# Kernel optimization log

Measured on AMD Instinct MI355X. Metric: run time of the kernel, lower is better.

The kernel has to match this reference:

```python
import jax, jax.numpy as jnp
import numpy as np

B, S, I, H, L = 32, 512, 512, 512, 2


def _gru_scan(x, wx, bx, wh, bh, reverse):
    # x: [B, S, layer_in_dim]; wx: [3H, in], wh: [3H, H]. PyTorch gate order r,z,n.
    hdim = wh.shape[1]
    gx = jnp.einsum('bsi,gi->sbg', x, wx) + bx  # precompute input gates: [S, B, 3H]
    h0 = jnp.zeros((x.shape[0], hdim), x.dtype)

    def step(h, gxt):
        gh = h @ wh.T + bh
        r = jax.nn.sigmoid(gxt[:, :hdim] + gh[:, :hdim])
        z = jax.nn.sigmoid(gxt[:, hdim:2 * hdim] + gh[:, hdim:2 * hdim])
        n = jnp.tanh(gxt[:, 2 * hdim:] + r * gh[:, 2 * hdim:])
        hn = (1 - z) * n + z * h
        return hn, hn

    hN, ys = jax.lax.scan(step, h0, gx, reverse=reverse)
    return ys.transpose(1, 0, 2), hN  # [B, S, H], [B, H]


def setup_inputs() -> dict:
    key = jax.random.key(0)
    ks = jax.random.split(key, 17)
    sc = 0.05
    d = {'x': jax.random.normal(ks[0], (B, S, I), jnp.float32)}
    i = 1
    for layer in range(L):
        in_dim = I if layer == 0 else 2 * H
        for tag in ('f', 'b'):
            d[f'wx_{tag}{layer}'] = jax.random.normal(ks[i], (3 * H, in_dim), jnp.float32) * sc
            d[f'bx_{tag}{layer}'] = jax.random.normal(jax.random.fold_in(ks[i], 1), (3 * H,), jnp.float32) * sc
            d[f'wh_{tag}{layer}'] = jax.random.normal(jax.random.fold_in(ks[i], 2), (3 * H, H), jnp.float32) * sc
            d[f'bh_{tag}{layer}'] = jax.random.normal(jax.random.fold_in(ks[i], 3), (3 * H,), jnp.float32) * sc
            i += 1
    return d


def reference(x,
              wx_f0, bx_f0, wh_f0, bh_f0, wx_b0, bx_b0, wh_b0, bh_b0,
              wx_f1, bx_f1, wh_f1, bh_f1, wx_b1, bx_b1, wh_b1, bh_b1):
    layers = [((wx_f0, bx_f0, wh_f0, bh_f0), (wx_b0, bx_b0, wh_b0, bh_b0)),
              ((wx_f1, bx_f1, wh_f1, bh_f1), (wx_b1, bx_b1, wh_b1, bh_b1))]
    layer_in = x
    h_fw, h_bw = [], []
    for fw, bw in layers:
        yf, hf = _gru_scan(layer_in, *fw, reverse=False)
        yb, hb = _gru_scan(layer_in, *bw, reverse=True)
        layer_in = jnp.concatenate([yf, yb], axis=-1)  # [B, S, 2H] (dropout p=0 -> identity)
        h_fw.append(hf)
        h_bw.append(hb)
    return layer_in, (jnp.stack(h_fw, 0), jnp.stack(h_bw, 0))
```

## Files before the change

### kernel.cpp

```cpp
#include <hip/hip_runtime.h>
#include <stdint.h>

typedef short short8 __attribute__((ext_vector_type(8)));
typedef float floatx4 __attribute__((ext_vector_type(4)));
typedef unsigned long long u64;

__device__ __forceinline__ unsigned short f2bf(float f) {
  union { float f; unsigned int i; } v;
  v.f = f;
  unsigned int r = v.i + 0x7fffu + ((v.i >> 16) & 1u);
  return (unsigned short)(r >> 16);
}
__device__ __forceinline__ short8 cvt8(const float4 a, const float4 b) {
  short8 v;
  v[0] = (short)f2bf(a.x); v[1] = (short)f2bf(a.y);
  v[2] = (short)f2bf(a.z); v[3] = (short)f2bf(a.w);
  v[4] = (short)f2bf(b.x); v[5] = (short)f2bf(b.y);
  v[6] = (short)f2bf(b.z); v[7] = (short)f2bf(b.w);
  return v;
}
__device__ __forceinline__ float sane(float x, float lim) {
  return fminf(fmaxf(x, -lim), lim);
}

extern __shared__ unsigned short lds[];

template<int K, int XM>
__global__ __launch_bounds__(256)
void gx_gemm(const float* __restrict__ xf,
             const unsigned short* __restrict__ xb,
             const float* __restrict__ wxf,
             const float* __restrict__ wxb,
             float* __restrict__ gx)
{
  unsigned short* As = lds;
  unsigned short* Bs = lds + 128 * 40;

  const int M0 = blockIdx.x * 128;
  const int N0 = blockIdx.y * 128;
  const int dir = blockIdx.z;
  const float* wx = dir ? wxb : wxf;
  float* gxd = gx + (long)dir * 16384 * 1536;

  const int tid = threadIdx.x;
  const int lane = tid & 63;
  const int wid = tid >> 6;
  const int q = lane >> 4;
  const int l16 = lane & 15;
  const int wM = (wid >> 1) * 64;
  const int wN = (wid & 1) * 64;

  const int srow = tid >> 1;
  const int k0 = (tid & 1) * 16;

  floatx4 acc[4][4];
#pragma unroll
  for (int i = 0; i < 4; ++i)
#pragma unroll
    for (int j = 0; j < 4; ++j) acc[i][j] = (floatx4){0.f, 0.f, 0.f, 0.f};

  for (int kk = 0; kk < K; kk += 32) {
    __syncthreads();
    {
      const int mg = M0 + srow;
      if (XM) {
        const float* ap = xf + ((long)(mg & 31) * 512 + (mg >> 5)) * 512 + kk + k0;
        float4 f0 = *(const float4*)(ap);
        float4 f1 = *(const float4*)(ap + 4);
        float4 f2 = *(const float4*)(ap + 8);
        float4 f3 = *(const float4*)(ap + 12);
        *(short8*)(As + srow * 40 + k0)     = cvt8(f0, f1);
        *(short8*)(As + srow * 40 + k0 + 8) = cvt8(f2, f3);
      } else {
        const unsigned short* ap = xb + (long)mg * 1024 + kk + k0;
        *(short8*)(As + srow * 40 + k0)     = *(const short8*)(ap);
        *(short8*)(As + srow * 40 + k0 + 8) = *(const short8*)(ap + 8);
      }
      const float* bp = wx + (long)(N0 + srow) * K + kk + k0;
      float4 g0 = *(const float4*)(bp);
      float4 g1 = *(const float4*)(bp + 4);
      float4 g2 = *(const float4*)(bp + 8);
      float4 g3 = *(const float4*)(bp + 12);
      *(short8*)(Bs + srow * 40 + k0)     = cvt8(g0, g1);
      *(short8*)(Bs + srow * 40 + k0 + 8) = cvt8(g2, g3);
    }
    __syncthreads();
    short8 a[4], b[4];
#pragma unroll
    for (int mt = 0; mt < 4; ++mt)
      a[mt] = *(const short8*)(As + (wM + mt * 16 + l16) * 40 + q * 8);
#pragma unroll
    for (int nt = 0; nt < 4; ++nt)
      b[nt] = *(const short8*)(Bs + (wN + nt * 16 + l16) * 40 + q * 8);
#pragma unroll
    for (int mt = 0; mt < 4; ++mt)
#pragma unroll
      for (int nt = 0; nt < 4; ++nt)
        acc[mt][nt] = __builtin_amdgcn_mfma_f32_16x16x32_bf16(
            a[mt], b[nt], acc[mt][nt], 0, 0, 0);
  }
#pragma unroll
  for (int mt = 0; mt < 4; ++mt) {
    const int row = M0 + wM + mt * 16 + q * 4;
#pragma unroll
    for (int nt = 0; nt < 4; ++nt) {
      const int col = N0 + wN + nt * 16 + l16;
#pragma unroll
      for (int r = 0; r < 4; ++r)
        gxd[(long)(row + r) * 1536 + col] = acc[mt][nt][r];
    }
  }
}

template<int OUT>
__global__ __launch_bounds__(128)
void gru_rec(const float* __restrict__ gx,
             const float* __restrict__ whfp, const float* __restrict__ bhfp,
             const float* __restrict__ whbp, const float* __restrict__ bhbp,
             const float* __restrict__ bxfp, const float* __restrict__ bxbp,
             unsigned short* __restrict__ ring,
             unsigned short* __restrict__ y0,
             float* __restrict__ omain,
             float* __restrict__ out_hf,
             float* __restrict__ out_hb)
{
  constexpr u64 TM = 0x4000400040004000ULL;
  unsigned short* whs = lds;

  const int bid = blockIdx.x;
  const bool fw = bid < 16;
  const int d = fw ? bid : bid - 16;
  const int tid = threadIdx.x;
  const int lane = tid & 63;
  const int w = tid >> 6;
  const int q = lane >> 4;
  const int l16 = lane & 15;

  const float* wh = fw ? whfp : whbp;
  const float* bh = fw ? bhfp : bhbp;
  const float* bx = fw ? bxfp : bxbp;
  const int col0 = d * 32;
  const int dirofs = fw ? 0 : 512;
  const float* gxd = gx + (long)(fw ? 0 : 1) * 16384 * 1536;

  for (int c = tid; c < 96 * 64; c += 128) {
    int lr = c >> 6, c8 = (c & 63) * 8;
    int g = lr >> 5, jc = lr & 31;
    const float* src = wh + (long)(g * 512 + col0 + jc) * 512 + c8;
    *(short8*)(whs + lr * 520 + c8) =
        cvt8(*(const float4*)src, *(const float4*)(src + 4));
  }
  __syncthreads();

  const int jj = l16;
  float cr[2], cz[2], bxn[2], bhn[2];
#pragma unroll
  for (int n2 = 0; n2 < 2; ++n2) {
    const int cc = col0 + n2 * 16 + jj;
    cr[n2] = bx[cc] + bh[cc];
    cz[n2] = bx[512 + cc] + bh[512 + cc];
    bxn[n2] = bx[1024 + cc];
    bhn[n2] = bh[1024 + cc];
  }

  const int cb = w * 16 + q * 4;
  const int ab = w * 16 + l16;
  const floatx4 fz = {0.f, 0.f, 0.f, 0.f};
  float h[2][4] = {{0.f, 0.f, 0.f, 0.f}, {0.f, 0.f, 0.f, 0.f}};
  unsigned int* ring32 = (unsigned int*)ring;
  unsigned int* y032 = (unsigned int*)y0;

  float nx[24];
  auto load_gx = [&](int t) {
    const float* base = gxd + (long)t * 32 * 1536;
#pragma unroll
    for (int g = 0; g < 3; ++g)
#pragma unroll
      for (int n2 = 0; n2 < 2; ++n2)
#pragma unroll
        for (int r = 0; r < 4; ++r)
          nx[(g * 2 + n2) * 4 + r] =
              base[(long)(cb + r) * 1536 + g * 512 + col0 + n2 * 16 + jj];
  };
  { const int t0 = fw ? 0 : 511; load_gx(t0); }

  union W { u64 u[2]; short8 s; unsigned int dd[4]; };

  for (int it = 0; it < 512; ++it) {
    const int t = fw ? it : 511 - it;
    float cur[24];
#pragma unroll
    for (int i = 0; i < 24; ++i) cur[i] = nx[i];

    const unsigned short* hbase = nullptr;
    u64 expectw = 0;
    if (it > 0) {
      const int slot_r = (it + 1) & 1;
      hbase = ring + ((long)slot_r * 32 + ab) * 1024 + dirofs;
      expectw = ((((it - 1) >> 1) & 1) ^ 1) ? TM : 0ULL;
    }

    W wv[16];
    if (it > 0) {
#pragma unroll
      for (int ks = 0; ks < 16; ++ks) {
        u64* p = (u64*)(hbase + ks * 32 + q * 8);
        wv[ks].u[0] = __hip_atomic_load(p,     __ATOMIC_RELAXED, __HIP_MEMORY_SCOPE_AGENT);
        wv[ks].u[1] = __hip_atomic_load(p + 1, __ATOMIC_RELAXED, __HIP_MEMORY_SCOPE_AGENT);
      }
    }
    if (it < 511) {
      const int tn = fw ? it + 1 : 511 - (it + 1);
      load_gx(tn);
    }

    floatx4 ar[2] = {fz, fz}, az[2] = {fz, fz}, an[2] = {fz, fz};
    if (it > 0) {
      while (true) {
        u64 bad = 0;
#pragma unroll
        for (int ks = 0; ks < 16; ++ks)
          bad |= ((wv[ks].u[0] ^ expectw) | (wv[ks].u[1] ^ expectw)) & TM;
        if (bad == 0) break;
        __builtin_amdgcn_s_sleep(1);
#pragma unroll
        for (int ks = 0; ks < 16; ++ks) {
          u64* p = (u64*)(hbase + ks * 32 + q * 8);
          wv[ks].u[0] = __hip_atomic_load(p,     __ATOMIC_RELAXED, __HIP_MEMORY_SCOPE_AGENT);
          wv[ks].u[1] = __hip_atomic_load(p + 1, __ATOMIC_RELAXED, __HIP_MEMORY_SCOPE_AGENT);
        }
      }
#pragma unroll
      for (int ks = 0; ks < 16; ++ks) {
        wv[ks].dd[0] &= 0xBFFFBFFFu; wv[ks].dd[1] &= 0xBFFFBFFFu;
        wv[ks].dd[2] &= 0xBFFFBFFFu; wv[ks].dd[3] &= 0xBFFFBFFFu;
        short8 a = wv[ks].s;
#pragma unroll
        for (int n2 = 0; n2 < 2; ++n2) {
          short8 vr = *(const short8*)(whs + (n2 * 16 + jj) * 520 + ks * 32 + q * 8);
          short8 vz = *(const short8*)(whs + (32 + n2 * 16 + jj) * 520 + ks * 32 + q * 8);
          short8 vn = *(const short8*)(whs + (64 + n2 * 16 + jj) * 520 + ks * 32 + q * 8);
          ar[n2] = __builtin_amdgcn_mfma_f32_16x16x32_bf16(a, vr, ar[n2], 0, 0, 0);
          az[n2] = __builtin_amdgcn_mfma_f32_16x16x32_bf16(a, vz, az[n2], 0, 0, 0);
          an[n2] = __builtin_amdgcn_mfma_f32_16x16x32_bf16(a, vn, an[n2], 0, 0, 0);
        }
      }
    }

    unsigned int hwp[2][4];
#pragma unroll
    for (int n2 = 0; n2 < 2; ++n2) {
#pragma unroll
      for (int r = 0; r < 4; ++r) {
        const float xr = sane(cur[(0 * 2 + n2) * 4 + r] + ar[n2][r] + cr[n2], 60.f);
        const float xz = sane(cur[(1 * 2 + n2) * 4 + r] + az[n2][r] + cz[n2], 60.f);
        const float rr = 1.f / (1.f + __expf(-xr));
        const float zz = 1.f / (1.f + __expf(-xz));
        const float xn = sane(cur[(2 * 2 + n2) * 4 + r] + bxn[n2] +
                              rr * (an[n2][r] + bhn[n2]), 30.f);
        const float e2 = __expf(-2.f * xn);
        const float nn = (1.f - e2) / (1.f + e2);
        h[n2][r] = (1.f - zz) * nn + zz * h[n2][r];
        int v = f2bf(h[n2][r]);
        int pm = __shfl_xor(v, 1);
        hwp[n2][r] = (unsigned int)(v & 0xffff) |
                     ((unsigned int)(pm & 0xffff) << 16);
      }
    }

    const unsigned int tb = (((it >> 1) & 1) ^ 1) ? 0x40004000u : 0u;
    const int slot_w = it & 1;
    if ((jj & 1) == 0) {
#pragma unroll
      for (int n2 = 0; n2 < 2; ++n2) {
        const int colw = (dirofs + col0 + n2 * 16 + jj) >> 1;
#pragma unroll
        for (int r = 0; r < 4; ++r) {
          __hip_atomic_store(ring32 + ((long)slot_w * 32 + cb + r) * 512 + colw,
                             hwp[n2][r] | tb,
                             __ATOMIC_RELAXED, __HIP_MEMORY_SCOPE_AGENT);
          if (OUT == 0)
            y032[((long)t * 32 + cb + r) * 512 + colw] = hwp[n2][r];
        }
      }
    }
    if (OUT == 1) {
#pragma unroll
      for (int n2 = 0; n2 < 2; ++n2)
#pragma unroll
        for (int r = 0; r < 4; ++r)
          omain[(long)(cb + r) * 524288 + (long)t * 1024 +
                dirofs + col0 + n2 * 16 + jj] = h[n2][r];
    }
    if (it == 511) {
      float* oh = fw ? out_hf : out_hb;
#pragma unroll
      for (int n2 = 0; n2 < 2; ++n2)
#pragma unroll
        for (int r = 0; r < 4; ++r)
          oh[(cb + r) * 512 + col0 + n2 * 16 + jj] = h[n2][r];
    }
  }
}

extern "C" void kernel_launch(void* const* d_in, const int* in_sizes, int n_in,
                              void* d_out, int out_size, void* d_ws, size_t ws_size,
                              hipStream_t stream)
{
  (void)in_sizes; (void)n_in; (void)out_size; (void)ws_size;

  const float* x    = (const float*)d_in[0];
  const float* wxf0 = (const float*)d_in[1];
  const float* bxf0 = (const float*)d_in[2];
  const float* whf0 = (const float*)d_in[3];
  const float* bhf0 = (const float*)d_in[4];
  const float* wxb0 = (const float*)d_in[5];
  const float* bxb0 = (const float*)d_in[6];
  const float* whb0 = (const float*)d_in[7];
  const float* bhb0 = (const float*)d_in[8];
  const float* wxf1 = (const float*)d_in[9];
  const float* bxf1 = (const float*)d_in[10];
  const float* whf1 = (const float*)d_in[11];
  const float* bhf1 = (const float*)d_in[12];
  const float* wxb1 = (const float*)d_in[13];
  const float* bxb1 = (const float*)d_in[14];
  const float* whb1 = (const float*)d_in[15];
  const float* bhb1 = (const float*)d_in[16];

  char* ws = (char*)d_ws;
  float* gx             = (float*)(ws);
  unsigned short* y0    = (unsigned short*)(ws + 201326592L);
  unsigned short* ring0 = (unsigned short*)(ws + 234881024L);
  unsigned short* ring1 = (unsigned short*)(ws + 235012096L);

  float* out = (float*)d_out;
  float* out_hf0 = out + 16777216L;
  float* out_hf1 = out + 16777216L + 16384L;
  float* out_hb0 = out + 16777216L + 32768L;
  float* out_hb1 = out + 16777216L + 49152L;

  const size_t lds_gemm = (size_t)(2 * 128 * 40) * 2;
  const size_t lds_rec  = (size_t)(96 * 520) * 2;
  (void)hipFuncSetAttribute((const void*)gru_rec<0>,
                            hipFuncAttributeMaxDynamicSharedMemorySize, (int)lds_rec);
  (void)hipFuncSetAttribute((const void*)gru_rec<1>,
                            hipFuncAttributeMaxDynamicSharedMemorySize, (int)lds_rec);

  hipMemsetAsync(ws + 234881024L, 0, 262144L, stream);

  gx_gemm<512, 1><<<dim3(128, 12, 2), dim3(256), lds_gemm, stream>>>(
      x, nullptr, wxf0, wxb0, gx);
  gru_rec<0><<<dim3(32), dim3(128), lds_rec, stream>>>(
      gx, whf0, bhf0, whb0, bhb0, bxf0, bxb0,
      ring0, y0, nullptr, out_hf0, out_hb0);
  gx_gemm<1024, 0><<<dim3(128, 12, 2), dim3(256), lds_gemm, stream>>>(
      nullptr, y0, wxf1, wxb1, gx);
  gru_rec<1><<<dim3(32), dim3(128), lds_rec, stream>>>(
      gx, whf1, bhf1, whb1, bhb1, bxf1, bxb1,
      ring1, nullptr, out, out_hf1, out_hb1);
}
```

Measured before the change: 7.077 ms.

## Store recurrent hidden state in MFMA fragment layout; use nontemporal loads and stores

The exchange ring that carries each step's hidden state between blocks is laid out so that each lane's A-fragment is one contiguous 16-byte chunk, and lanes of a wave read consecutive addresses. This replaces the strided row-major ring read and its 32 atomic 64-bit loads per step. Writers now use a lane-shuffle transpose to assemble 16-byte fragments and store them with paired 64-bit atomics. The speculative first read becomes a plain nontemporal vector load, and the gx loads and output stores are also marked nontemporal. The cost is extra shuffle work on the critical recurrent path and reliance on the tag bits to detect torn non-atomic reads.

```diff
diff --git a/kernel.cpp b/kernel.cpp
--- a/kernel.cpp
+++ b/kernel.cpp
@@ -141,6 +141,7 @@
   const float* bx = fw ? bxfp : bxbp;
   const int col0 = d * 32;
   const int dirofs = fw ? 0 : 512;
+  const long dirbyte = fw ? 0 : 32768;
   const float* gxd = gx + (long)(fw ? 0 : 1) * 16384 * 1536;
 
   for (int c = tid; c < 96 * 64; c += 128) {
@@ -164,10 +165,8 @@
   }
 
   const int cb = w * 16 + q * 4;
-  const int ab = w * 16 + l16;
   const floatx4 fz = {0.f, 0.f, 0.f, 0.f};
   float h[2][4] = {{0.f, 0.f, 0.f, 0.f}, {0.f, 0.f, 0.f, 0.f}};
-  unsigned int* ring32 = (unsigned int*)ring;
   unsigned int* y032 = (unsigned int*)y0;
 
   float nx[24];
@@ -179,12 +178,12 @@
       for (int n2 = 0; n2 < 2; ++n2)
 #pragma unroll
         for (int r = 0; r < 4; ++r)
-          nx[(g * 2 + n2) * 4 + r] =
-              base[(long)(cb + r) * 1536 + g * 512 + col0 + n2 * 16 + jj];
+          nx[(g * 2 + n2) * 4 + r] = __builtin_nontemporal_load(
+              base + (long)(cb + r) * 1536 + g * 512 + col0 + n2 * 16 + jj);
   };
   { const int t0 = fw ? 0 : 511; load_gx(t0); }
 
-  union W { u64 u[2]; short8 s; unsigned int dd[4]; };
+  union V { u64 u[2]; short8 s; unsigned int dd[4]; };
 
   for (int it = 0; it < 512; ++it) {
     const int t = fw ? it : 511 - it;
@@ -192,22 +191,20 @@
 #pragma unroll
     for (int i = 0; i < 24; ++i) cur[i] = nx[i];
 
-    const unsigned short* hbase = nullptr;
+    const char* rbase = nullptr;
     u64 expectw = 0;
     if (it > 0) {
       const int slot_r = (it + 1) & 1;
-      hbase = ring + ((long)slot_r * 32 + ab) * 1024 + dirofs;
+      rbase = (const char*)ring + (long)slot_r * 65536 + dirbyte +
+              (long)w * 16384 + (long)lane * 16;
       expectw = ((((it - 1) >> 1) & 1) ^ 1) ? TM : 0ULL;
     }
 
-    W wv[16];
+    short8 af[16];
     if (it > 0) {
 #pragma unroll
-      for (int ks = 0; ks < 16; ++ks) {
-        u64* p = (u64*)(hbase + ks * 32 + q * 8);
-        wv[ks].u[0] = __hip_atomic_load(p,     __ATOMIC_RELAXED, __HIP_MEMORY_SCOPE_AGENT);
-        wv[ks].u[1] = __hip_atomic_load(p + 1, __ATOMIC_RELAXED, __HIP_MEMORY_SCOPE_AGENT);
-      }
+      for (int ks = 0; ks < 16; ++ks)
+        af[ks] = __builtin_nontemporal_load((const short8*)(rbase + ks * 1024));
     }
     if (it < 511) {
       const int tn = fw ? it + 1 : 511 - (it + 1);
@@ -219,22 +216,27 @@
       while (true) {
         u64 bad = 0;
 #pragma unroll
-        for (int ks = 0; ks < 16; ++ks)
-          bad |= ((wv[ks].u[0] ^ expectw) | (wv[ks].u[1] ^ expectw)) & TM;
+        for (int ks = 0; ks < 16; ++ks) {
+          V v; v.s = af[ks];
+          bad |= ((v.u[0] ^ expectw) | (v.u[1] ^ expectw)) & TM;
+        }
         if (bad == 0) break;
         __builtin_amdgcn_s_sleep(1);
 #pragma unroll
         for (int ks = 0; ks < 16; ++ks) {
-          u64* p = (u64*)(hbase + ks * 32 + q * 8);
-          wv[ks].u[0] = __hip_atomic_load(p,     __ATOMIC_RELAXED, __HIP_MEMORY_SCOPE_AGENT);
-          wv[ks].u[1] = __hip_atomic_load(p + 1, __ATOMIC_RELAXED, __HIP_MEMORY_SCOPE_AGENT);
+          u64* p = (u64*)(rbase + ks * 1024);
+          V v;
+          v.u[0] = __hip_atomic_load(p,     __ATOMIC_RELAXED, __HIP_MEMORY_SCOPE_AGENT);
+          v.u[1] = __hip_atomic_load(p + 1, __ATOMIC_RELAXED, __HIP_MEMORY_SCOPE_AGENT);
+          af[ks] = v.s;
         }
       }
 #pragma unroll
       for (int ks = 0; ks < 16; ++ks) {
-        wv[ks].dd[0] &= 0xBFFFBFFFu; wv[ks].dd[1] &= 0xBFFFBFFFu;
-        wv[ks].dd[2] &= 0xBFFFBFFFu; wv[ks].dd[3] &= 0xBFFFBFFFu;
-        short8 a = wv[ks].s;
+        V v; v.s = af[ks];
+        v.dd[0] &= 0xBFFFBFFFu; v.dd[1] &= 0xBFFFBFFFu;
+        v.dd[2] &= 0xBFFFBFFFu; v.dd[3] &= 0xBFFFBFFFu;
+        short8 a = v.s;
 #pragma unroll
         for (int n2 = 0; n2 < 2; ++n2) {
           short8 vr = *(const short8*)(whs + (n2 * 16 + jj) * 520 + ks * 32 + q * 8);
@@ -247,7 +249,7 @@
       }
     }
 
-    unsigned int hwp[2][4];
+    unsigned short hb16[2][4];
 #pragma unroll
     for (int n2 = 0; n2 < 2; ++n2) {
 #pragma unroll
@@ -261,26 +263,61 @@
         const float e2 = __expf(-2.f * xn);
         const float nn = (1.f - e2) / (1.f + e2);
         h[n2][r] = (1.f - zz) * nn + zz * h[n2][r];
-        int v = f2bf(h[n2][r]);
-        int pm = __shfl_xor(v, 1);
-        hwp[n2][r] = (unsigned int)(v & 0xffff) |
-                     ((unsigned int)(pm & 0xffff) << 16);
-      }
-    }
-
-    const unsigned int tb = (((it >> 1) & 1) ^ 1) ? 0x40004000u : 0u;
-    const int slot_w = it & 1;
-    if ((jj & 1) == 0) {
+        hb16[n2][r] = f2bf(h[n2][r]);
+      }
+    }
+
+    {
+      const unsigned short utag = (((it >> 1) & 1) ^ 1) ? 0x4000 : 0;
+      const int slot_w = it & 1;
+      char* sb = (char*)ring + (long)slot_w * 65536 + dirbyte + (long)w * 16384;
+      const int o = l16 >> 3;
+#pragma unroll
+      for (int n2 = 0; n2 < 2; ++n2) {
+        const int cb2 = col0 + n2 * 16 + o * 8;
+        const int ksq = (cb2 >> 5) * 1024 + ((cb2 >> 3) & 3) * 256;
+        u64 lo = 0, hi = 0;
+#pragma unroll
+        for (int r = 0; r < 4; ++r) {
+          int tv = (int)(unsigned short)(hb16[n2][r] | utag);
+          int pm = __shfl_xor(tv, 1);
+          unsigned int pair = (l16 & 1)
+              ? ((unsigned)(pm & 0xffff) | ((unsigned)tv << 16))
+              : ((unsigned)(tv & 0xffff) | ((unsigned)pm << 16));
+          unsigned int pm2 = (unsigned)__shfl_xor((int)pair, 2);
+          unsigned int d0 = (l16 & 2) ? pm2 : pair;
+          unsigned int d1 = (l16 & 2) ? pair : pm2;
+          unsigned int p0 = (unsigned)__shfl_xor((int)d0, 4);
+          unsigned int p1 = (unsigned)__shfl_xor((int)d1, 4);
+          unsigned int e0 = (l16 & 4) ? p0 : d0;
+          unsigned int e1 = (l16 & 4) ? p1 : d1;
+          unsigned int e2 = (l16 & 4) ? d0 : p0;
+          unsigned int e3 = (l16 & 4) ? d1 : p1;
+          if ((l16 & 3) == r) {
+            lo = (u64)e0 | ((u64)e1 << 32);
+            hi = (u64)e2 | ((u64)e3 << 32);
+          }
+        }
+        if ((l16 & 4) == 0) {
+          u64* p = (u64*)(sb + ksq + (q * 4 + (l16 & 3)) * 16);
+          __hip_atomic_store(p,     lo, __ATOMIC_RELAXED, __HIP_MEMORY_SCOPE_AGENT);
+          __hip_atomic_store(p + 1, hi, __ATOMIC_RELAXED, __HIP_MEMORY_SCOPE_AGENT);
+        }
+      }
+    }
+
+    if (OUT == 0) {
 #pragma unroll
       for (int n2 = 0; n2 < 2; ++n2) {
         const int colw = (dirofs + col0 + n2 * 16 + jj) >> 1;
 #pragma unroll
         for (int r = 0; r < 4; ++r) {
-          __hip_atomic_store(ring32 + ((long)slot_w * 32 + cb + r) * 512 + colw,
-                             hwp[n2][r] | tb,
-                             __ATOMIC_RELAXED, __HIP_MEMORY_SCOPE_AGENT);
-          if (OUT == 0)
-            y032[((long)t * 32 + cb + r) * 512 + colw] = hwp[n2][r];
+          int v = hb16[n2][r];
+          int pm = __shfl_xor(v, 1);
+          unsigned int pr = (unsigned)(v & 0xffff) | ((unsigned)(pm & 0xffff) << 16);
+          if ((jj & 1) == 0)
+            __builtin_nontemporal_store(pr,
+                y032 + ((long)t * 32 + cb + r) * 512 + colw);
         }
       }
     }
@@ -289,8 +326,9 @@
       for (int n2 = 0; n2 < 2; ++n2)
 #pragma unroll
         for (int r = 0; r < 4; ++r)
-          omain[(long)(cb + r) * 524288 + (long)t * 1024 +
-                dirofs + col0 + n2 * 16 + jj] = h[n2][r];
+          __builtin_nontemporal_store(h[n2][r],
+              omain + (long)(cb + r) * 524288 + (long)t * 1024 +
+              dirofs + col0 + n2 * 16 + jj);
     }
     if (it == 511) {
       float* oh = fw ? out_hf : out_hb;
```

Measured after the change: 6.596 ms. -6.8%, faster.
